# Kernel tuning notes

Measured on AMD Instinct MI355X. Metric: run time of the kernel, lower is better.

The kernel has to match this reference:

```python
import jax, jax.numpy as jnp
import numpy as np

N_NODES = 100000
N_EDGES = 1600000
IN, HID, OUT = 128, 128, 64


def setup_inputs() -> dict:
    key = jax.random.key(0)
    ks = jax.random.split(key, 12)
    x = jax.random.normal(ks[0], (N_NODES, IN), dtype=jnp.float32)
    src = jax.random.randint(ks[1], (N_EDGES,), 0, N_NODES, dtype=jnp.int32)
    dst = jax.random.randint(ks[2], (N_EDGES,), 0, N_NODES, dtype=jnp.int32)

    def lin(k, fan_in, fan_out):
        return jax.random.normal(k, (fan_in, fan_out), dtype=jnp.float32) / jnp.sqrt(jnp.float32(fan_in))

    return {
        "x": x, "src": src, "dst": dst,
        "w_self_0": lin(ks[3], IN, HID), "w_neigh_0": lin(ks[4], IN, HID), "b_0": jnp.zeros((HID,), jnp.float32),
        "w_self_1": lin(ks[5], HID, HID), "w_neigh_1": lin(ks[6], HID, HID), "b_1": jnp.zeros((HID,), jnp.float32),
        "w_self_2": lin(ks[7], HID, OUT), "w_neigh_2": lin(ks[8], HID, OUT), "b_2": jnp.zeros((OUT,), jnp.float32),
    }


def reference(x, src, dst, w_self_0, w_neigh_0, b_0, w_self_1, w_neigh_1, b_1, w_self_2, w_neigh_2, b_2):
    n = x.shape[0]
    # in-degree per dst node; zero-degree nodes keep aggregated 0 (clamp avoids div-by-0)
    deg = jax.ops.segment_sum(jnp.ones_like(dst, dtype=x.dtype), dst, num_segments=n)
    inv_deg = (1.0 / jnp.maximum(deg, 1.0))[:, None]

    def sage_layer(h, w_s, w_n, b):
        # irregular gather of src features, segment-mean over dst
        agg = jax.ops.segment_sum(h[src], dst, num_segments=n) * inv_deg
        return h @ w_s + agg @ w_n + b

    h = jax.nn.relu(sage_layer(x, w_self_0, w_neigh_0, b_0))   # dropout = identity (eval)
    h = jax.nn.relu(sage_layer(h, w_self_1, w_neigh_1, b_1))
    return sage_layer(h, w_self_2, w_neigh_2, b_2)
```

## Files before the change

kernel.cpp:

```cpp
#include <hip/hip_runtime.h>


#define NN 100000
#define NE 1600000
#define BSH 7
#define BND 128
#define NB  782
#define NBLKS 256
#define EPB ((NE + NBLKS - 1) / NBLKS)
#define STOT (NB * NBLKS)
#define NSB ((STOT + 1023) / 1024)
#define GEMM_BLOCKS 1563

typedef __attribute__((ext_vector_type(8))) short short8;
typedef __attribute__((ext_vector_type(4))) float f32x4;
typedef unsigned int uint;
typedef unsigned short ushort;

__device__ inline ushort f2bf(float f) {
    uint u = __float_as_uint(f);
    u += 0x7FFFu + ((u >> 16) & 1u);
    return (ushort)(u >> 16);
}
__device__ inline float bf_lo(uint w) { return __uint_as_float(w << 16); }
__device__ inline float bf_hi(uint w) { return __uint_as_float(w & 0xFFFF0000u); }

template<int NCS, int NCN, bool XF32, bool ABF>
__device__ void gemm_body(int bid, int tid,
    const void* __restrict__ Hv, const ushort* __restrict__ Wf,
    const float* __restrict__ bias, void* __restrict__ Av, ushort* __restrict__ Bt)
{
    constexpr int NCT = (NCS + NCN) / 16;
    const int g = (bid * 256 + tid) >> 6;
    if (g >= NN / 16) return;
    const int lane = tid & 63;
    const int m = lane & 15;
    const int q = lane >> 4;

    short8 af[4];
    if (XF32) {
        const float* hp = (const float*)Hv + (size_t)(g * 16 + m) * 128;
        #pragma unroll
        for (int kt = 0; kt < 4; ++kt) {
            const float4 f0 = *(const float4*)(hp + kt * 32 + q * 8);
            const float4 f1 = *(const float4*)(hp + kt * 32 + q * 8 + 4);
            short8 v;
            v[0] = (short)f2bf(f0.x); v[1] = (short)f2bf(f0.y);
            v[2] = (short)f2bf(f0.z); v[3] = (short)f2bf(f0.w);
            v[4] = (short)f2bf(f1.x); v[5] = (short)f2bf(f1.y);
            v[6] = (short)f2bf(f1.z); v[7] = (short)f2bf(f1.w);
            af[kt] = v;
        }
    } else {
        const short8* hp = (const short8*)((const ushort*)Hv + (size_t)(g * 16 + m) * 128);
        #pragma unroll
        for (int kt = 0; kt < 4; ++kt) af[kt] = hp[kt * 4 + q];
    }

    f32x4 acc[NCT];
    #pragma unroll
    for (int i = 0; i < NCT; ++i) acc[i] = (f32x4){0.f, 0.f, 0.f, 0.f};

    const short8* wp = (const short8*)Wf;
    #pragma unroll
    for (int ct = 0; ct < NCT; ++ct) {
        #pragma unroll
        for (int kt = 0; kt < 4; ++kt) {
            const short8 bf = wp[(ct * 4 + kt) * 64 + lane];
            acc[ct] = __builtin_amdgcn_mfma_f32_16x16x32_bf16(af[kt], bf, acc[ct], 0, 0, 0);
        }
    }

    const int r0 = g * 16 + q * 4;
    #pragma unroll
    for (int ct = 0; ct < NCS / 16; ++ct) {
        const int c = ct * 16 + m;
        const float bv = bias[c];
        #pragma unroll
        for (int r = 0; r < 4; ++r) {
            const float v = acc[ct][r] + bv;
            if (ABF) ((ushort*)Av)[(size_t)(r0 + r) * NCS + c] = f2bf(v);
            else     ((float*) Av)[(size_t)(r0 + r) * NCS + c] = v;
        }
    }
    #pragma unroll
    for (int ct = NCS / 16; ct < NCT; ++ct) {
        const int c = ct * 16 + m - NCS;
        #pragma unroll
        for (int r = 0; r < 4; ++r)
            Bt[(size_t)(r0 + r) * NCN + c] = f2bf(acc[ct][r]);
    }
}

template<int NCS, int NCN, bool XF32, bool ABF>
__global__ __launch_bounds__(256) void gemm_mfma_k(
    const void* __restrict__ Hv, const ushort* __restrict__ Wf,
    const float* __restrict__ bias, void* __restrict__ Av, ushort* __restrict__ Bt)
{
    gemm_body<NCS, NCN, XF32, ABF>(blockIdx.x, threadIdx.x, Hv, Wf, bias, Av, Bt);
}

__global__ __launch_bounds__(256) void phist_pack_k(
    const int* __restrict__ dst, int* __restrict__ histG,
    const float* __restrict__ ws0, const float* __restrict__ wn0, ushort* __restrict__ wf0,
    const float* __restrict__ ws1, const float* __restrict__ wn1, ushort* __restrict__ wf1,
    const float* __restrict__ ws2, const float* __restrict__ wn2, ushort* __restrict__ wf2)
{
    __shared__ int h[NB];
    const int t = threadIdx.x;
    if (blockIdx.x < NBLKS) {
        for (int i = t; i < NB; i += 256) h[i] = 0;
        __syncthreads();
        const int blk = blockIdx.x;
        const int e0 = blk * EPB;
        const int e1 = min(e0 + EPB, NE);
        for (int e = e0 + t; e < e1; e += 256)
            atomicAdd(&h[dst[e] >> BSH], 1);
        __syncthreads();
        for (int i = t; i < NB; i += 256)
            histG[i * NBLKS + blk] = h[i];
        return;
    }
    const int b = blockIdx.x - NBLKS;
    const float *ws, *wn; ushort* wf; int ncs, idx;
    if (b < 16)      { ws = ws0; wn = wn0; wf = wf0; ncs = 128; idx = b * 256 + t; }
    else if (b < 32) { ws = ws1; wn = wn1; wf = wf1; ncs = 128; idx = (b - 16) * 256 + t; }
    else             { ws = ws2; wn = wn2; wf = wf2; ncs = 64;  idx = (b - 32) * 256 + t; }
    const int total = (2 * ncs / 16) * 4 * 64;
    if (idx >= total) return;
    const int l = idx & 63;
    const int f = idx >> 6;
    const int kt = f & 3;
    const int ct = f >> 2;
    const int n = ct * 16 + (l & 15);
    const int k0 = kt * 32 + (l >> 4) * 8;
    uint w[4];
    #pragma unroll
    for (int p = 0; p < 4; ++p) {
        const int k = k0 + p * 2;
        float v0, v1;
        if (n < ncs) { v0 = ws[k * ncs + n];         v1 = ws[(k + 1) * ncs + n]; }
        else         { v0 = wn[k * ncs + (n - ncs)]; v1 = wn[(k + 1) * ncs + (n - ncs)]; }
        w[p] = (uint)f2bf(v0) | ((uint)f2bf(v1) << 16);
    }
    uint4 o; o.x = w[0]; o.y = w[1]; o.z = w[2]; o.w = w[3];
    ((uint4*)wf)[idx] = o;
}

__global__ __launch_bounds__(256) void scan1_k(int* __restrict__ data, int* __restrict__ blksum) {
    __shared__ int lds[256];
    const int t = threadIdx.x;
    const int base = blockIdx.x * 1024 + t * 4;
    int v[4];
    #pragma unroll
    for (int i = 0; i < 4; ++i) {
        const int idx = base + i;
        v[i] = (idx < STOT) ? data[idx] : 0;
    }
    const int s = v[0] + v[1] + v[2] + v[3];
    lds[t] = s;
    __syncthreads();
    #pragma unroll
    for (int off = 1; off < 256; off <<= 1) {
        const int cur = lds[t];
        const int y = (t >= off) ? lds[t - off] : 0;
        __syncthreads();
        lds[t] = cur + y;
        __syncthreads();
    }
    const int incl = lds[t];
    if (t == 255) blksum[blockIdx.x] = incl;
    int run = incl - s;
    #pragma unroll
    for (int i = 0; i < 4; ++i) {
        const int idx = base + i;
        if (idx < STOT) data[idx] = run;
        run += v[i];
    }
}

__global__ __launch_bounds__(256) void scan3_k(int* __restrict__ data, const int* __restrict__ blksum) {
    __shared__ int lds[256];
    const int t = threadIdx.x;
    lds[t] = (t < NSB) ? blksum[t] : 0;
    __syncthreads();
    #pragma unroll
    for (int off = 1; off < 256; off <<= 1) {
        const int cur = lds[t];
        const int y = (t >= off) ? lds[t - off] : 0;
        __syncthreads();
        lds[t] = cur + y;
        __syncthreads();
    }
    const int add = (blockIdx.x == 0) ? 0 : lds[blockIdx.x - 1];
    const int base = blockIdx.x * 1024 + t * 4;
    #pragma unroll
    for (int i = 0; i < 4; ++i) {
        const int idx = base + i;
        if (idx < STOT) data[idx] += add;
    }
}

__global__ __launch_bounds__(256) void pscatter_gemm0_k(
    const int* __restrict__ src, const int* __restrict__ dst,
    const int* __restrict__ histG, int* __restrict__ pb,
    const float* __restrict__ x, const ushort* __restrict__ wf0,
    const float* __restrict__ b0, ushort* __restrict__ Abf, ushort* __restrict__ Bt)
{
    __shared__ int wc[NB];
    const int t = threadIdx.x;
    if (blockIdx.x < NBLKS) {
        const int blk = blockIdx.x;
        for (int i = t; i < NB; i += 256) wc[i] = histG[i * NBLKS + blk];
        __syncthreads();
        const int e0 = blk * EPB;
        const int e1 = min(e0 + EPB, NE);
        for (int e = e0 + t; e < e1; e += 256) {
            const int d = dst[e];
            const int pos = atomicAdd(&wc[d >> BSH], 1);
            pb[pos] = (src[e] << BSH) | (d & (BND - 1));
        }
        return;
    }
    gemm_body<128, 128, true, true>(blockIdx.x - NBLKS, t, x, wf0, b0, Abf, Bt);
}

__global__ __launch_bounds__(256) void bucket_place_k(const int* __restrict__ histG,
                                                      const int* __restrict__ pb,
                                                      int* __restrict__ row,
                                                      int* __restrict__ esrc) {
    __shared__ int cnt[BND], wc[BND], excl[BND], scan[BND];
    const int b = blockIdx.x;
    const int t = threadIdx.x;
    if (t < BND) { cnt[t] = 0; wc[t] = 0; }
    __syncthreads();
    const int s0 = histG[b * NBLKS];
    const int s1 = (b + 1 < NB) ? histG[(b + 1) * NBLKS] : NE;
    for (int e = s0 + t; e < s1; e += 256)
        atomicAdd(&cnt[pb[e] & (BND - 1)], 1);
    __syncthreads();
    if (t < BND) scan[t] = cnt[t];
    __syncthreads();
    for (int off = 1; off < BND; off <<= 1) {
        int nv = 0;
        if (t < BND) {
            nv = scan[t];
            if (t >= off) nv += scan[t - off];
        }
        __syncthreads();
        if (t < BND) scan[t] = nv;
        __syncthreads();
    }
    if (t < BND) {
        const int ex = scan[t] - cnt[t];
        excl[t] = ex;
        const int node = b * BND + t;
        if (node <= NN) row[node] = s0 + ex;
    }
    __syncthreads();
    for (int e = s0 + t; e < s1; e += 256) {
        const int p = pb[e];
        const int dl = p & (BND - 1);
        const int pos = s0 + excl[dl] + atomicAdd(&wc[dl], 1);
        esrc[pos] = p >> BSH;
    }
}

__global__ __launch_bounds__(256) void agg128_k(
    const int* __restrict__ row, const int* __restrict__ esrc,
    const ushort* __restrict__ Bt, const ushort* __restrict__ Abf, ushort* __restrict__ Hb)
{
    const int w = (blockIdx.x * 256 + threadIdx.x) >> 6;
    const int half = (threadIdx.x >> 5) & 1;
    const int ln = threadIdx.x & 31;
    const int node = w * 2 + half;
    if (node >= NN) return;
    const int e0 = row[node];
    const int e1 = row[node + 1];
    const uint2* B = (const uint2*)Bt;
    float a0 = 0.f, a1 = 0.f, a2 = 0.f, a3 = 0.f;
    int e = e0;
    for (; e + 8 <= e1; e += 8) {
        int s[8];
        #pragma unroll
        for (int j = 0; j < 8; ++j) s[j] = esrc[e + j];
        uint2 v[8];
        #pragma unroll
        for (int j = 0; j < 8; ++j) v[j] = B[(size_t)s[j] * 32 + ln];
        #pragma unroll
        for (int j = 0; j < 8; ++j) {
            a0 += bf_lo(v[j].x); a1 += bf_hi(v[j].x);
            a2 += bf_lo(v[j].y); a3 += bf_hi(v[j].y);
        }
    }
    for (; e + 2 <= e1; e += 2) {
        const int s0 = esrc[e], s1 = esrc[e + 1];
        const uint2 v0 = B[(size_t)s0 * 32 + ln];
        const uint2 v1 = B[(size_t)s1 * 32 + ln];
        a0 += bf_lo(v0.x) + bf_lo(v1.x); a1 += bf_hi(v0.x) + bf_hi(v1.x);
        a2 += bf_lo(v0.y) + bf_lo(v1.y); a3 += bf_hi(v0.y) + bf_hi(v1.y);
    }
    if (e < e1) {
        const uint2 v = B[(size_t)esrc[e] * 32 + ln];
        a0 += bf_lo(v.x); a1 += bf_hi(v.x);
        a2 += bf_lo(v.y); a3 += bf_hi(v.y);
    }
    const int deg = e1 - e0;
    const float invd = (deg > 0) ? 1.0f / (float)deg : 0.0f;
    const uint2 aw = ((const uint2*)Abf)[(size_t)node * 32 + ln];
    const float v0 = fmaxf(bf_lo(aw.x) + a0 * invd, 0.f);
    const float v1 = fmaxf(bf_hi(aw.x) + a1 * invd, 0.f);
    const float v2 = fmaxf(bf_lo(aw.y) + a2 * invd, 0.f);
    const float v3 = fmaxf(bf_hi(aw.y) + a3 * invd, 0.f);
    uint2 o;
    o.x = (uint)f2bf(v0) | ((uint)f2bf(v1) << 16);
    o.y = (uint)f2bf(v2) | ((uint)f2bf(v3) << 16);
    ((uint2*)Hb)[(size_t)node * 32 + ln] = o;
}

__global__ __launch_bounds__(256) void agg64_k(
    const int* __restrict__ row, const int* __restrict__ esrc,
    const ushort* __restrict__ Bt, float* __restrict__ out)
{
    const int node = (blockIdx.x * 256 + threadIdx.x) >> 4;
    const int ln = threadIdx.x & 15;
    if (node >= NN) return;
    const int e0 = row[node];
    const int e1 = row[node + 1];
    const uint2* B = (const uint2*)Bt;
    float a0 = 0.f, a1 = 0.f, a2 = 0.f, a3 = 0.f;
    int e = e0;
    for (; e + 8 <= e1; e += 8) {
        int s[8];
        #pragma unroll
        for (int j = 0; j < 8; ++j) s[j] = esrc[e + j];
        uint2 v[8];
        #pragma unroll
        for (int j = 0; j < 8; ++j) v[j] = B[(size_t)s[j] * 16 + ln];
        #pragma unroll
        for (int j = 0; j < 8; ++j) {
            a0 += bf_lo(v[j].x); a1 += bf_hi(v[j].x);
            a2 += bf_lo(v[j].y); a3 += bf_hi(v[j].y);
        }
    }
    for (; e + 2 <= e1; e += 2) {
        const int s0 = esrc[e], s1 = esrc[e + 1];
        const uint2 v0 = B[(size_t)s0 * 16 + ln];
        const uint2 v1 = B[(size_t)s1 * 16 + ln];
        a0 += bf_lo(v0.x) + bf_lo(v1.x); a1 += bf_hi(v0.x) + bf_hi(v1.x);
        a2 += bf_lo(v0.y) + bf_lo(v1.y); a3 += bf_hi(v0.y) + bf_hi(v1.y);
    }
    if (e < e1) {
        const uint2 v = B[(size_t)esrc[e] * 16 + ln];
        a0 += bf_lo(v.x); a1 += bf_hi(v.x);
        a2 += bf_lo(v.y); a3 += bf_hi(v.y);
    }
    const int deg = e1 - e0;
    const float invd = (deg > 0) ? 1.0f / (float)deg : 0.0f;
    float4* op = (float4*)(out + (size_t)node * 64 + ln * 4);
    float4 o = *op;
    o.x += a0 * invd; o.y += a1 * invd;
    o.z += a2 * invd; o.w += a3 * invd;
    *op = o;
}

__device__ inline float4 relu4f(float4 v) {
    v.x = fmaxf(v.x, 0.f); v.y = fmaxf(v.y, 0.f);
    v.z = fmaxf(v.z, 0.f); v.w = fmaxf(v.w, 0.f);
    return v;
}
template<int NCOL, bool RELU_IN, bool BIAS>
__global__ __launch_bounds__(256) void gemm_k(
    const float* in, const float* __restrict__ W,
    const float* __restrict__ bias, float* out)
{
    constexpr int K = 128;
    constexpr int QUADS = NCOL / 4;
    constexpr int G = 256 / QUADS;
    constexpr int RPT = 32 / G;
    __shared__ float Wlds[K * NCOL];
    {
        const float4* Wg = reinterpret_cast<const float4*>(W);
        float4* Wl = reinterpret_cast<float4*>(Wlds);
        #pragma unroll
        for (int i = 0; i < K * NCOL / 4 / 256; ++i)
            Wl[threadIdx.x + i * 256] = Wg[threadIdx.x + i * 256];
    }
    __syncthreads();
    const int tx = threadIdx.x % QUADS;
    const int ty = threadIdx.x / QUADS;
    const int row0 = blockIdx.x * 32;
    const float* rp[RPT];
    #pragma unroll
    for (int i = 0; i < RPT; ++i) rp[i] = in + (size_t)(row0 + ty + i * G) * K;
    float acc[RPT][4];
    #pragma unroll
    for (int i = 0; i < RPT; ++i) acc[i][0] = acc[i][1] = acc[i][2] = acc[i][3] = 0.f;
    #pragma unroll 2
    for (int kc = 0; kc < K; kc += 4) {
        float4 h4[RPT];
        #pragma unroll
        for (int i = 0; i < RPT; ++i) {
            h4[i] = *reinterpret_cast<const float4*>(rp[i] + kc);
            if (RELU_IN) h4[i] = relu4f(h4[i]);
        }
        #pragma unroll
        for (int kk = 0; kk < 4; ++kk) {
            const float4 w4 = *reinterpret_cast<const float4*>(&Wlds[(kc + kk) * NCOL + tx * 4]);
            #pragma unroll
            for (int i = 0; i < RPT; ++i) {
                const float hv = (&h4[i].x)[kk];
                acc[i][0] = fmaf(hv, w4.x, acc[i][0]);
                acc[i][1] = fmaf(hv, w4.y, acc[i][1]);
                acc[i][2] = fmaf(hv, w4.z, acc[i][2]);
                acc[i][3] = fmaf(hv, w4.w, acc[i][3]);
            }
        }
    }
    float4 b4 = make_float4(0.f, 0.f, 0.f, 0.f);
    if (BIAS) b4 = *reinterpret_cast<const float4*>(&bias[tx * 4]);
    #pragma unroll
    for (int i = 0; i < RPT; ++i) {
        const int r = row0 + ty + i * G;
        float4 o;
        o.x = acc[i][0] + b4.x; o.y = acc[i][1] + b4.y;
        o.z = acc[i][2] + b4.z; o.w = acc[i][3] + b4.w;
        *reinterpret_cast<float4*>(&out[(size_t)r * NCOL + tx * 4]) = o;
    }
}
__global__ void deg_k(const int* __restrict__ dst, float* __restrict__ deg, int E) {
    const int i = blockIdx.x * blockDim.x + threadIdx.x;
    if (i < E) atomicAdd(&deg[dst[i]], 1.0f);
}
__global__ void inv_k(float* deg, int n) {
    const int i = blockIdx.x * blockDim.x + threadIdx.x;
    if (i < n) deg[i] = 1.0f / fmaxf(deg[i], 1.0f);
}
__global__ __launch_bounds__(256) void scatter128_k(
    const int* __restrict__ src, const int* __restrict__ dst,
    const float* __restrict__ inv, const float* __restrict__ B, float* A, int E) {
    const int lane = threadIdx.x & 63;
    int w = (blockIdx.x * 256 + threadIdx.x) >> 6;
    const int nw = (gridDim.x * 256) >> 6;
    for (int e = w; e < E; e += nw) {
        const int s = src[e], d = dst[e];
        const float sc = inv[d];
        const float2 v = *reinterpret_cast<const float2*>(&B[(size_t)s * 128 + lane * 2]);
        atomicAdd(&A[(size_t)d * 128 + lane * 2    ], v.x * sc);
        atomicAdd(&A[(size_t)d * 128 + lane * 2 + 1], v.y * sc);
    }
}
__global__ __launch_bounds__(256) void scatter64_k(
    const int* __restrict__ src, const int* __restrict__ dst,
    const float* __restrict__ inv, const float* __restrict__ B, float* A, int E) {
    const int lane = threadIdx.x & 63;
    int w = (blockIdx.x * 256 + threadIdx.x) >> 6;
    const int nw = (gridDim.x * 256) >> 6;
    for (int e = w; e < E; e += nw) {
        const int s = src[e], d = dst[e];
        atomicAdd(&A[(size_t)d * 64 + lane], B[(size_t)s * 64 + lane] * inv[d]);
    }
}

extern "C" void kernel_launch(void* const* d_in, const int* in_sizes, int n_in,
                              void* d_out, int out_size, void* d_ws, size_t ws_size,
                              hipStream_t stream) {
    const float* x   = (const float*)d_in[0];
    const int*   src = (const int*)  d_in[1];
    const int*   dst = (const int*)  d_in[2];
    const float* ws0 = (const float*)d_in[3];
    const float* wn0 = (const float*)d_in[4];
    const float* b0  = (const float*)d_in[5];
    const float* ws1 = (const float*)d_in[6];
    const float* wn1 = (const float*)d_in[7];
    const float* b1  = (const float*)d_in[8];
    const float* ws2 = (const float*)d_in[9];
    const float* wn2 = (const float*)d_in[10];
    const float* b2  = (const float*)d_in[11];
    float* out = (float*)d_out;

    const size_t O_BLK  = 4096;
    const size_t O_ROW  = 16384;
    const size_t O_WF0  = 417792;
    const size_t O_WF1  = 483328;
    const size_t O_WF2  = 548864;
    const size_t O_ESRC = 581632;
    const size_t O_PB   = 6983680;
    const size_t O_HIST = 13385728;
    const size_t O_A    = 14286848;
    const size_t O_BT   = 39890944;
    const size_t O_HB   = 65495040;
    const size_t NEED   = 91095040;

    if (ws_size >= NEED) {
        int*    blks  = (int*)   ((char*)d_ws + O_BLK);
        int*    row   = (int*)   ((char*)d_ws + O_ROW);
        ushort* wf0   = (ushort*)((char*)d_ws + O_WF0);
        ushort* wf1   = (ushort*)((char*)d_ws + O_WF1);
        ushort* wf2   = (ushort*)((char*)d_ws + O_WF2);
        int*    esrc  = (int*)   ((char*)d_ws + O_ESRC);
        int*    pb    = (int*)   ((char*)d_ws + O_PB);
        int*    histG = (int*)   ((char*)d_ws + O_HIST);
        ushort* Abf   = (ushort*)((char*)d_ws + O_A);
        ushort* Bt    = (ushort*)((char*)d_ws + O_BT);
        ushort* Hb    = (ushort*)((char*)d_ws + O_HB);

        phist_pack_k<<<NBLKS + 40, 256, 0, stream>>>(dst, histG,
            ws0, wn0, wf0, ws1, wn1, wf1, ws2, wn2, wf2);
        scan1_k<<<NSB, 256, 0, stream>>>(histG, blks);
        scan3_k<<<NSB, 256, 0, stream>>>(histG, blks);
        pscatter_gemm0_k<<<NBLKS + GEMM_BLOCKS, 256, 0, stream>>>(
            src, dst, histG, pb, x, wf0, b0, Abf, Bt);
        bucket_place_k<<<NB, 256, 0, stream>>>(histG, pb, row, esrc);

        const int AGG128_BLOCKS = (NN / 2 + 3) / 4;
        const int AGG64_BLOCKS  = (NN + 63) / 64;
        const int A64B = (NN + 15) / 16;

        agg128_k<<<AGG128_BLOCKS, 256, 0, stream>>>(row, esrc, Bt, Abf, Hb);
        gemm_mfma_k<128, 128, false, true ><<<GEMM_BLOCKS, 256, 0, stream>>>(Hb, wf1, b1, Abf, Bt);
        agg128_k<<<AGG128_BLOCKS, 256, 0, stream>>>(row, esrc, Bt, Abf, Hb);
        gemm_mfma_k<64, 64, false, false><<<GEMM_BLOCKS, 256, 0, stream>>>(Hb, wf2, b2, out, Bt);
        agg64_k<<<A64B, 256, 0, stream>>>(row, esrc, Bt, out);
        (void)AGG64_BLOCKS;
    } else {
        float* inv = (float*)d_ws;
        float* H0  = (float*)((char*)d_ws + (1u << 20));
        float* Bf  = H0 + (size_t)NN * 128;
        const int GB = NN / 32;
        const int SC_BLOCKS = 4096;
        hipMemsetAsync(inv, 0, NN * sizeof(float), stream);
        deg_k<<<(NE + 255) / 256, 256, 0, stream>>>(dst, inv, NE);
        inv_k<<<(NN + 255) / 256, 256, 0, stream>>>(inv, NN);
        gemm_k<128, false, false><<<GB, 256, 0, stream>>>(x, wn0, nullptr, Bf);
        gemm_k<128, false, true ><<<GB, 256, 0, stream>>>(x, ws0, b0, H0);
        scatter128_k<<<SC_BLOCKS, 256, 0, stream>>>(src, dst, inv, Bf, H0, NE);
        gemm_k<128, true, false><<<GB, 256, 0, stream>>>(H0, wn1, nullptr, Bf);
        gemm_k<128, true, true ><<<GB, 256, 0, stream>>>(H0, ws1, b1, H0);
        scatter128_k<<<SC_BLOCKS, 256, 0, stream>>>(src, dst, inv, Bf, H0, NE);
        gemm_k<64, true, false><<<GB, 256, 0, stream>>>(H0, wn2, nullptr, Bf);
        gemm_k<64, true, true ><<<GB, 256, 0, stream>>>(H0, ws2, b2, out);
        scatter64_k<<<SC_BLOCKS, 256, 0, stream>>>(src, dst, inv, Bf, out, NE);
    }
}
```

Baseline: 394.5 us.

## Build CSR via per-node atomic degree count and scatter, stage GEMM weights in LDS

```diff
diff --git a/kernel.cpp b/kernel.cpp
--- a/kernel.cpp
+++ b/kernel.cpp
@@ -3,14 +3,12 @@
 
 #define NN 100000
 #define NE 1600000
-#define BSH 7
-#define BND 128
-#define NB  782
+#define ND1 (NN + 1)
 #define NBLKS 256
 #define EPB ((NE + NBLKS - 1) / NBLKS)
-#define STOT (NB * NBLKS)
-#define NSB ((STOT + 1023) / 1024)
-#define GEMM_BLOCKS 1563
+#define SCAN_E 2048
+#define NSBD ((ND1 + SCAN_E - 1) / SCAN_E)
+#define GEMM0_BLOCKS 782
 
 typedef __attribute__((ext_vector_type(8))) short short8;
 typedef __attribute__((ext_vector_type(4))) float f32x4;
@@ -26,20 +24,19 @@
 __device__ inline float bf_hi(uint w) { return __uint_as_float(w & 0xFFFF0000u); }
 
 template<int NCS, int NCN, bool XF32, bool ABF>
-__device__ void gemm_body(int bid, int tid,
-    const void* __restrict__ Hv, const ushort* __restrict__ Wf,
+__device__ void gemm_body(int wid, int tid,
+    const void* __restrict__ Hv, const short8* __restrict__ wp,
     const float* __restrict__ bias, void* __restrict__ Av, ushort* __restrict__ Bt)
 {
     constexpr int NCT = (NCS + NCN) / 16;
-    const int g = (bid * 256 + tid) >> 6;
-    if (g >= NN / 16) return;
+    if (wid >= NN / 16) return;
     const int lane = tid & 63;
     const int m = lane & 15;
     const int q = lane >> 4;
 
     short8 af[4];
     if (XF32) {
-        const float* hp = (const float*)Hv + (size_t)(g * 16 + m) * 128;
+        const float* hp = (const float*)Hv + (size_t)(wid * 16 + m) * 128;
         #pragma unroll
         for (int kt = 0; kt < 4; ++kt) {
             const float4 f0 = *(const float4*)(hp + kt * 32 + q * 8);
@@ -52,7 +49,7 @@
             af[kt] = v;
         }
     } else {
-        const short8* hp = (const short8*)((const ushort*)Hv + (size_t)(g * 16 + m) * 128);
+        const short8* hp = (const short8*)((const ushort*)Hv + (size_t)(wid * 16 + m) * 128);
         #pragma unroll
         for (int kt = 0; kt < 4; ++kt) af[kt] = hp[kt * 4 + q];
     }
@@ -61,7 +58,6 @@
     #pragma unroll
     for (int i = 0; i < NCT; ++i) acc[i] = (f32x4){0.f, 0.f, 0.f, 0.f};
 
-    const short8* wp = (const short8*)Wf;
     #pragma unroll
     for (int ct = 0; ct < NCT; ++ct) {
         #pragma unroll
@@ -71,7 +67,7 @@
         }
     }
 
-    const int r0 = g * 16 + q * 4;
+    const int r0 = wid * 16 + q * 4;
     #pragma unroll
     for (int ct = 0; ct < NCS / 16; ++ct) {
         const int c = ct * 16 + m;
@@ -93,32 +89,33 @@
 }
 
 template<int NCS, int NCN, bool XF32, bool ABF>
-__global__ __launch_bounds__(256) void gemm_mfma_k(
+__global__ __launch_bounds__(512) void gemm_mfma_k(
     const void* __restrict__ Hv, const ushort* __restrict__ Wf,
     const float* __restrict__ bias, void* __restrict__ Av, ushort* __restrict__ Bt)
 {
-    gemm_body<NCS, NCN, XF32, ABF>(blockIdx.x, threadIdx.x, Hv, Wf, bias, Av, Bt);
-}
-
-__global__ __launch_bounds__(256) void phist_pack_k(
-    const int* __restrict__ dst, int* __restrict__ histG,
+    constexpr int NCT = (NCS + NCN) / 16;
+    __shared__ short8 wl[NCT * 4 * 64];
+    uint4* dl = (uint4*)wl;
+    const uint4* sg = (const uint4*)Wf;
+    for (int i = threadIdx.x; i < NCT * 4 * 64; i += 512) dl[i] = sg[i];
+    __syncthreads();
+    gemm_body<NCS, NCN, XF32, ABF>(
+        (blockIdx.x * 512 + threadIdx.x) >> 6, threadIdx.x, Hv, wl, bias, Av, Bt);
+}
+
+__global__ __launch_bounds__(256) void dhist_pack_k(
+    const int* __restrict__ dst, int* __restrict__ deg,
     const float* __restrict__ ws0, const float* __restrict__ wn0, ushort* __restrict__ wf0,
     const float* __restrict__ ws1, const float* __restrict__ wn1, ushort* __restrict__ wf1,
     const float* __restrict__ ws2, const float* __restrict__ wn2, ushort* __restrict__ wf2)
 {
-    __shared__ int h[NB];
     const int t = threadIdx.x;
     if (blockIdx.x < NBLKS) {
-        for (int i = t; i < NB; i += 256) h[i] = 0;
-        __syncthreads();
         const int blk = blockIdx.x;
         const int e0 = blk * EPB;
         const int e1 = min(e0 + EPB, NE);
         for (int e = e0 + t; e < e1; e += 256)
-            atomicAdd(&h[dst[e] >> BSH], 1);
-        __syncthreads();
-        for (int i = t; i < NB; i += 256)
-            histG[i * NBLKS + blk] = h[i];
+            atomicAdd(&deg[dst[e]], 1);
         return;
     }
     const int b = blockIdx.x - NBLKS;
@@ -150,14 +147,15 @@
 __global__ __launch_bounds__(256) void scan1_k(int* __restrict__ data, int* __restrict__ blksum) {
     __shared__ int lds[256];
     const int t = threadIdx.x;
-    const int base = blockIdx.x * 1024 + t * 4;
-    int v[4];
-    #pragma unroll
-    for (int i = 0; i < 4; ++i) {
+    const int base = blockIdx.x * SCAN_E + t * 8;
+    int v[8];
+    int s = 0;
+    #pragma unroll
+    for (int i = 0; i < 8; ++i) {
         const int idx = base + i;
-        v[i] = (idx < STOT) ? data[idx] : 0;
-    }
-    const int s = v[0] + v[1] + v[2] + v[3];
+        v[i] = (idx < ND1) ? data[idx] : 0;
+        s += v[i];
+    }
     lds[t] = s;
     __syncthreads();
     #pragma unroll
@@ -172,98 +170,76 @@
     if (t == 255) blksum[blockIdx.x] = incl;
     int run = incl - s;
     #pragma unroll
-    for (int i = 0; i < 4; ++i) {
+    for (int i = 0; i < 8; ++i) {
         const int idx = base + i;
-        if (idx < STOT) data[idx] = run;
+        if (idx < ND1) data[idx] = run;
         run += v[i];
     }
 }
 
-__global__ __launch_bounds__(256) void scan3_k(int* __restrict__ data, const int* __restrict__ blksum) {
+__global__ __launch_bounds__(256) void scan3_k(int* __restrict__ data,
+                                               const int* __restrict__ blksum,
+                                               int* __restrict__ cur) {
     __shared__ int lds[256];
     const int t = threadIdx.x;
-    lds[t] = (t < NSB) ? blksum[t] : 0;
+    lds[t] = (t < NSBD) ? blksum[t] : 0;
     __syncthreads();
     #pragma unroll
     for (int off = 1; off < 256; off <<= 1) {
-        const int cur = lds[t];
+        const int c = lds[t];
         const int y = (t >= off) ? lds[t - off] : 0;
         __syncthreads();
-        lds[t] = cur + y;
+        lds[t] = c + y;
         __syncthreads();
     }
     const int add = (blockIdx.x == 0) ? 0 : lds[blockIdx.x - 1];
-    const int base = blockIdx.x * 1024 + t * 4;
-    #pragma unroll
-    for (int i = 0; i < 4; ++i) {
+    const int base = blockIdx.x * SCAN_E + t * 8;
+    #pragma unroll
+    for (int i = 0; i < 8; ++i) {
         const int idx = base + i;
-        if (idx < STOT) data[idx] += add;
-    }
-}
-
-__global__ __launch_bounds__(256) void pscatter_gemm0_k(
+        if (idx < ND1) {
+            const int v = data[idx] + add;
+            data[idx] = v;
+            cur[idx] = v;
+        }
+    }
+}
+
+__global__ __launch_bounds__(512) void dscatter_gemm0_k(
     const int* __restrict__ src, const int* __restrict__ dst,
-    const int* __restrict__ histG, int* __restrict__ pb,
+    int* __restrict__ cur, int* __restrict__ esrc,
     const float* __restrict__ x, const ushort* __restrict__ wf0,
     const float* __restrict__ b0, ushort* __restrict__ Abf, ushort* __restrict__ Bt)
 {
-    __shared__ int wc[NB];
+    __shared__ uint4 sh[4096];
     const int t = threadIdx.x;
     if (blockIdx.x < NBLKS) {
         const int blk = blockIdx.x;
-        for (int i = t; i < NB; i += 256) wc[i] = histG[i * NBLKS + blk];
-        __syncthreads();
         const int e0 = blk * EPB;
         const int e1 = min(e0 + EPB, NE);
-        for (int e = e0 + t; e < e1; e += 256) {
+        int e = e0 + t;
+        for (; e + 1536 < e1; e += 2048) {
+            int d[4], s[4];
+            #pragma unroll
+            for (int j = 0; j < 4; ++j) { d[j] = dst[e + j * 512]; s[j] = src[e + j * 512]; }
+            int p[4];
+            #pragma unroll
+            for (int j = 0; j < 4; ++j) p[j] = atomicAdd(&cur[d[j]], 1);
+            #pragma unroll
+            for (int j = 0; j < 4; ++j) esrc[p[j]] = s[j];
+        }
+        for (; e < e1; e += 512) {
             const int d = dst[e];
-            const int pos = atomicAdd(&wc[d >> BSH], 1);
-            pb[pos] = (src[e] << BSH) | (d & (BND - 1));
+            const int pos = atomicAdd(&cur[d], 1);
+            esrc[pos] = src[e];
         }
         return;
     }
-    gemm_body<128, 128, true, true>(blockIdx.x - NBLKS, t, x, wf0, b0, Abf, Bt);
-}
-
-__global__ __launch_bounds__(256) void bucket_place_k(const int* __restrict__ histG,
-                                                      const int* __restrict__ pb,
-                                                      int* __restrict__ row,
-                                                      int* __restrict__ esrc) {
-    __shared__ int cnt[BND], wc[BND], excl[BND], scan[BND];
-    const int b = blockIdx.x;
-    const int t = threadIdx.x;
-    if (t < BND) { cnt[t] = 0; wc[t] = 0; }
+    const uint4* sg = (const uint4*)wf0;
+    for (int i = t; i < 4096; i += 512) sh[i] = sg[i];
     __syncthreads();
-    const int s0 = histG[b * NBLKS];
-    const int s1 = (b + 1 < NB) ? histG[(b + 1) * NBLKS] : NE;
-    for (int e = s0 + t; e < s1; e += 256)
-        atomicAdd(&cnt[pb[e] & (BND - 1)], 1);
-    __syncthreads();
-    if (t < BND) scan[t] = cnt[t];
-    __syncthreads();
-    for (int off = 1; off < BND; off <<= 1) {
-        int nv = 0;
-        if (t < BND) {
-            nv = scan[t];
-            if (t >= off) nv += scan[t - off];
-        }
-        __syncthreads();
-        if (t < BND) scan[t] = nv;
-        __syncthreads();
-    }
-    if (t < BND) {
-        const int ex = scan[t] - cnt[t];
-        excl[t] = ex;
-        const int node = b * BND + t;
-        if (node <= NN) row[node] = s0 + ex;
-    }
-    __syncthreads();
-    for (int e = s0 + t; e < s1; e += 256) {
-        const int p = pb[e];
-        const int dl = p & (BND - 1);
-        const int pos = s0 + excl[dl] + atomicAdd(&wc[dl], 1);
-        esrc[pos] = p >> BSH;
-    }
+    gemm_body<128, 128, true, true>(
+        ((blockIdx.x - NBLKS) * 512 + t) >> 6, t, x, (const short8*)sh, b0, Abf, Bt);
 }
 
 __global__ __launch_bounds__(256) void agg128_k(
@@ -485,8 +461,7 @@
     const size_t O_WF1  = 483328;
     const size_t O_WF2  = 548864;
     const size_t O_ESRC = 581632;
-    const size_t O_PB   = 6983680;
-    const size_t O_HIST = 13385728;
+    const size_t O_CUR  = 6983680;
     const size_t O_A    = 14286848;
     const size_t O_BT   = 39890944;
     const size_t O_HB   = 65495040;
@@ -499,30 +474,28 @@
         ushort* wf1   = (ushort*)((char*)d_ws + O_WF1);
         ushort* wf2   = (ushort*)((char*)d_ws + O_WF2);
         int*    esrc  = (int*)   ((char*)d_ws + O_ESRC);
-        int*    pb    = (int*)   ((char*)d_ws + O_PB);
-        int*    histG = (int*)   ((char*)d_ws + O_HIST);
+        int*    cur   = (int*)   ((char*)d_ws + O_CUR);
         ushort* Abf   = (ushort*)((char*)d_ws + O_A);
         ushort* Bt    = (ushort*)((char*)d_ws + O_BT);
         ushort* Hb    = (ushort*)((char*)d_ws + O_HB);
 
-        phist_pack_k<<<NBLKS + 40, 256, 0, stream>>>(dst, histG,
+        hipMemsetAsync(row, 0, (size_t)ND1 * 4, stream);
+        dhist_pack_k<<<NBLKS + 40, 256, 0, stream>>>(dst, row,
             ws0, wn0, wf0, ws1, wn1, wf1, ws2, wn2, wf2);
-        scan1_k<<<NSB, 256, 0, stream>>>(histG, blks);
-        scan3_k<<<NSB, 256, 0, stream>>>(histG, blks);
-        pscatter_gemm0_k<<<NBLKS + GEMM_BLOCKS, 256, 0, stream>>>(
-            src, dst, histG, pb, x, wf0, b0, Abf, Bt);
-        bucket_place_k<<<NB, 256, 0, stream>>>(histG, pb, row, esrc);
+        scan1_k<<<NSBD, 256, 0, stream>>>(row, blks);
+        scan3_k<<<NSBD, 256, 0, stream>>>(row, blks, cur);
+        dscatter_gemm0_k<<<NBLKS + GEMM0_BLOCKS, 512, 0, stream>>>(
+            src, dst, cur, esrc, x, wf0, b0, Abf, Bt);
 
         const int AGG128_BLOCKS = (NN / 2 + 3) / 4;
-        const int AGG64_BLOCKS  = (NN + 63) / 64;
         const int A64B = (NN + 15) / 16;
+        const int GEMM512_BLOCKS = (NN / 16 + 7) / 8;
 
         agg128_k<<<AGG128_BLOCKS, 256, 0, stream>>>(row, esrc, Bt, Abf, Hb);
-        gemm_mfma_k<128, 128, false, true ><<<GEMM_BLOCKS, 256, 0, stream>>>(Hb, wf1, b1, Abf, Bt);
+        gemm_mfma_k<128, 128, false, true ><<<GEMM512_BLOCKS, 512, 0, stream>>>(Hb, wf1, b1, Abf, Bt);
         agg128_k<<<AGG128_BLOCKS, 256, 0, stream>>>(row, esrc, Bt, Abf, Hb);
-        gemm_mfma_k<64, 64, false, false><<<GEMM_BLOCKS, 256, 0, stream>>>(Hb, wf2, b2, out, Bt);
+        gemm_mfma_k<64, 64, false, false><<<GEMM512_BLOCKS, 512, 0, stream>>>(Hb, wf2, b2, out, Bt);
         agg64_k<<<A64B, 256, 0, stream>>>(row, esrc, Bt, out);
-        (void)AGG64_BLOCKS;
     } else {
         float* inv = (float*)d_ws;
         float* H0  = (float*)((char*)d_ws + (1u << 20));
```

After: 514.8 us. 30.5% more time.

## Stage GEMM weight fragments in LDS with 512-thread blocks; widen scan per-thread work

Applied to the files above, without the earlier changes.

```diff
diff --git a/kernel.cpp b/kernel.cpp
--- a/kernel.cpp
+++ b/kernel.cpp
@@ -9,8 +9,9 @@
 #define NBLKS 256
 #define EPB ((NE + NBLKS - 1) / NBLKS)
 #define STOT (NB * NBLKS)
-#define NSB ((STOT + 1023) / 1024)
-#define GEMM_BLOCKS 1563
+#define SCAN_E 2048
+#define NSB ((STOT + SCAN_E - 1) / SCAN_E)
+#define GEMM0_BLOCKS 782
 
 typedef __attribute__((ext_vector_type(8))) short short8;
 typedef __attribute__((ext_vector_type(4))) float f32x4;
@@ -26,20 +27,19 @@
 __device__ inline float bf_hi(uint w) { return __uint_as_float(w & 0xFFFF0000u); }
 
 template<int NCS, int NCN, bool XF32, bool ABF>
-__device__ void gemm_body(int bid, int tid,
-    const void* __restrict__ Hv, const ushort* __restrict__ Wf,
+__device__ void gemm_body(int wid, int tid,
+    const void* __restrict__ Hv, const short8* __restrict__ wp,
     const float* __restrict__ bias, void* __restrict__ Av, ushort* __restrict__ Bt)
 {
     constexpr int NCT = (NCS + NCN) / 16;
-    const int g = (bid * 256 + tid) >> 6;
-    if (g >= NN / 16) return;
+    if (wid >= NN / 16) return;
     const int lane = tid & 63;
     const int m = lane & 15;
     const int q = lane >> 4;
 
     short8 af[4];
     if (XF32) {
-        const float* hp = (const float*)Hv + (size_t)(g * 16 + m) * 128;
+        const float* hp = (const float*)Hv + (size_t)(wid * 16 + m) * 128;
         #pragma unroll
         for (int kt = 0; kt < 4; ++kt) {
             const float4 f0 = *(const float4*)(hp + kt * 32 + q * 8);
@@ -52,7 +52,7 @@
             af[kt] = v;
         }
     } else {
-        const short8* hp = (const short8*)((const ushort*)Hv + (size_t)(g * 16 + m) * 128);
+        const short8* hp = (const short8*)((const ushort*)Hv + (size_t)(wid * 16 + m) * 128);
         #pragma unroll
         for (int kt = 0; kt < 4; ++kt) af[kt] = hp[kt * 4 + q];
     }
@@ -61,7 +61,6 @@
     #pragma unroll
     for (int i = 0; i < NCT; ++i) acc[i] = (f32x4){0.f, 0.f, 0.f, 0.f};
 
-    const short8* wp = (const short8*)Wf;
     #pragma unroll
     for (int ct = 0; ct < NCT; ++ct) {
         #pragma unroll
@@ -71,7 +70,7 @@
         }
     }
 
-    const int r0 = g * 16 + q * 4;
+    const int r0 = wid * 16 + q * 4;
     #pragma unroll
     for (int ct = 0; ct < NCS / 16; ++ct) {
         const int c = ct * 16 + m;
@@ -93,11 +92,18 @@
 }
 
 template<int NCS, int NCN, bool XF32, bool ABF>
-__global__ __launch_bounds__(256) void gemm_mfma_k(
+__global__ __launch_bounds__(512) void gemm_mfma_k(
     const void* __restrict__ Hv, const ushort* __restrict__ Wf,
     const float* __restrict__ bias, void* __restrict__ Av, ushort* __restrict__ Bt)
 {
-    gemm_body<NCS, NCN, XF32, ABF>(blockIdx.x, threadIdx.x, Hv, Wf, bias, Av, Bt);
+    constexpr int NCT = (NCS + NCN) / 16;
+    __shared__ short8 wl[NCT * 4 * 64];
+    uint4* dl = (uint4*)wl;
+    const uint4* sg = (const uint4*)Wf;
+    for (int i = threadIdx.x; i < NCT * 4 * 64; i += 512) dl[i] = sg[i];
+    __syncthreads();
+    gemm_body<NCS, NCN, XF32, ABF>(
+        (blockIdx.x * 512 + threadIdx.x) >> 6, threadIdx.x, Hv, wl, bias, Av, Bt);
 }
 
 __global__ __launch_bounds__(256) void phist_pack_k(
@@ -150,14 +156,15 @@
 __global__ __launch_bounds__(256) void scan1_k(int* __restrict__ data, int* __restrict__ blksum) {
     __shared__ int lds[256];
     const int t = threadIdx.x;
-    const int base = blockIdx.x * 1024 + t * 4;
-    int v[4];
-    #pragma unroll
-    for (int i = 0; i < 4; ++i) {
+    const int base = blockIdx.x * SCAN_E + t * 8;
+    int v[8];
+    int s = 0;
+    #pragma unroll
+    for (int i = 0; i < 8; ++i) {
         const int idx = base + i;
         v[i] = (idx < STOT) ? data[idx] : 0;
-    }
-    const int s = v[0] + v[1] + v[2] + v[3];
+        s += v[i];
+    }
     lds[t] = s;
     __syncthreads();
     #pragma unroll
@@ -172,7 +179,7 @@
     if (t == 255) blksum[blockIdx.x] = incl;
     int run = incl - s;
     #pragma unroll
-    for (int i = 0; i < 4; ++i) {
+    for (int i = 0; i < 8; ++i) {
         const int idx = base + i;
         if (idx < STOT) data[idx] = run;
         run += v[i];
@@ -193,36 +200,41 @@
         __syncthreads();
     }
     const int add = (blockIdx.x == 0) ? 0 : lds[blockIdx.x - 1];
-    const int base = blockIdx.x * 1024 + t * 4;
-    #pragma unroll
-    for (int i = 0; i < 4; ++i) {
+    const int base = blockIdx.x * SCAN_E + t * 8;
+    #pragma unroll
+    for (int i = 0; i < 8; ++i) {
         const int idx = base + i;
         if (idx < STOT) data[idx] += add;
     }
 }
 
-__global__ __launch_bounds__(256) void pscatter_gemm0_k(
+__global__ __launch_bounds__(512) void pscatter_gemm0_k(
     const int* __restrict__ src, const int* __restrict__ dst,
     const int* __restrict__ histG, int* __restrict__ pb,
     const float* __restrict__ x, const ushort* __restrict__ wf0,
     const float* __restrict__ b0, ushort* __restrict__ Abf, ushort* __restrict__ Bt)
 {
-    __shared__ int wc[NB];
+    __shared__ uint4 sh[4096];
     const int t = threadIdx.x;
     if (blockIdx.x < NBLKS) {
+        int* wc = (int*)sh;
         const int blk = blockIdx.x;
-        for (int i = t; i < NB; i += 256) wc[i] = histG[i * NBLKS + blk];
+        for (int i = t; i < NB; i += 512) wc[i] = histG[i * NBLKS + blk];
         __syncthreads();
         const int e0 = blk * EPB;
         const int e1 = min(e0 + EPB, NE);
-        for (int e = e0 + t; e < e1; e += 256) {
+        for (int e = e0 + t; e < e1; e += 512) {
             const int d = dst[e];
             const int pos = atomicAdd(&wc[d >> BSH], 1);
             pb[pos] = (src[e] << BSH) | (d & (BND - 1));
         }
         return;
     }
-    gemm_body<128, 128, true, true>(blockIdx.x - NBLKS, t, x, wf0, b0, Abf, Bt);
+    const uint4* sg = (const uint4*)wf0;
+    for (int i = t; i < 4096; i += 512) sh[i] = sg[i];
+    __syncthreads();
+    gemm_body<128, 128, true, true>(
+        ((blockIdx.x - NBLKS) * 512 + t) >> 6, t, x, (const short8*)sh, b0, Abf, Bt);
 }
 
 __global__ __launch_bounds__(256) void bucket_place_k(const int* __restrict__ histG,
@@ -486,7 +498,6 @@
     const size_t O_WF2  = 548864;
     const size_t O_ESRC = 581632;
     const size_t O_PB   = 6983680;
-    const size_t O_HIST = 13385728;
     const size_t O_A    = 14286848;
     const size_t O_BT   = 39890944;
     const size_t O_HB   = 65495040;
@@ -500,29 +511,28 @@
         ushort* wf2   = (ushort*)((char*)d_ws + O_WF2);
         int*    esrc  = (int*)   ((char*)d_ws + O_ESRC);
         int*    pb    = (int*)   ((char*)d_ws + O_PB);
-        int*    histG = (int*)   ((char*)d_ws + O_HIST);
         ushort* Abf   = (ushort*)((char*)d_ws + O_A);
         ushort* Bt    = (ushort*)((char*)d_ws + O_BT);
         ushort* Hb    = (ushort*)((char*)d_ws + O_HB);
+        int*    histG = (int*)   ((char*)d_ws + O_HB);
 
         phist_pack_k<<<NBLKS + 40, 256, 0, stream>>>(dst, histG,
             ws0, wn0, wf0, ws1, wn1, wf1, ws2, wn2, wf2);
         scan1_k<<<NSB, 256, 0, stream>>>(histG, blks);
         scan3_k<<<NSB, 256, 0, stream>>>(histG, blks);
-        pscatter_gemm0_k<<<NBLKS + GEMM_BLOCKS, 256, 0, stream>>>(
+        pscatter_gemm0_k<<<NBLKS + GEMM0_BLOCKS, 512, 0, stream>>>(
             src, dst, histG, pb, x, wf0, b0, Abf, Bt);
         bucket_place_k<<<NB, 256, 0, stream>>>(histG, pb, row, esrc);
 
         const int AGG128_BLOCKS = (NN / 2 + 3) / 4;
-        const int AGG64_BLOCKS  = (NN + 63) / 64;
         const int A64B = (NN + 15) / 16;
+        const int GEMM512_BLOCKS = (NN / 16 + 7) / 8;
 
         agg128_k<<<AGG128_BLOCKS, 256, 0, stream>>>(row, esrc, Bt, Abf, Hb);
-        gemm_mfma_k<128, 128, false, true ><<<GEMM_BLOCKS, 256, 0, stream>>>(Hb, wf1, b1, Abf, Bt);
+        gemm_mfma_k<128, 128, false, true ><<<GEMM512_BLOCKS, 512, 0, stream>>>(Hb, wf1, b1, Abf, Bt);
         agg128_k<<<AGG128_BLOCKS, 256, 0, stream>>>(row, esrc, Bt, Abf, Hb);
-        gemm_mfma_k<64, 64, false, false><<<GEMM_BLOCKS, 256, 0, stream>>>(Hb, wf2, b2, out, Bt);
+        gemm_mfma_k<64, 64, false, false><<<GEMM512_BLOCKS, 512, 0, stream>>>(Hb, wf2, b2, out, Bt);
         agg64_k<<<A64B, 256, 0, stream>>>(row, esrc, Bt, out);
-        (void)AGG64_BLOCKS;
     } else {
         float* inv = (float*)d_ws;
         float* H0  = (float*)((char*)d_ws + (1u << 20));
```

New measurement: 360.1 us. 1.1x faster.
